# Optimization experiments

Hardware: AMD Instinct MI355X
Metric: run time of the kernel (lower is better)

## Reference

```python
import jax, jax.numpy as jnp
import numpy as np

EPS = 1e-5

def setup_inputs() -> dict:
    key = jax.random.key(0)
    ks = jax.random.split(key, 6)
    B, S, F, D = 512, 64, 768, 256
    # xavier-ish scales for weights
    return {
        "audio_feat": jax.random.normal(ks[0], (B, S, F), dtype=jnp.float32),
        "visual_feat": jax.random.normal(ks[1], (B, S, F), dtype=jnp.float32),
        "Wa": jax.random.normal(ks[2], (F, D), dtype=jnp.float32) * (1.0 / np.sqrt(F)),
        "ba": jnp.zeros((D,), dtype=jnp.float32),
        "Wv": jax.random.normal(ks[3], (F, D), dtype=jnp.float32) * (1.0 / np.sqrt(F)),
        "bv": jnp.zeros((D,), dtype=jnp.float32),
        "corr": jax.random.normal(ks[4], (D, D), dtype=jnp.float32) * float(np.sqrt(2.0 / (D + D))),
        "Wb": jax.random.normal(ks[5], (2 * D, 64), dtype=jnp.float32) * (1.0 / np.sqrt(2 * D)),
        "bb": jnp.zeros((64,), dtype=jnp.float32),
        "gamma": jnp.ones((64,), dtype=jnp.float32),
        "beta": jnp.zeros((64,), dtype=jnp.float32),
    }


def reference(audio_feat, visual_feat, Wa, ba, Wv, bv, corr, Wb, bb, gamma, beta):
    # project: [b,s,768] -> [b,s,256]
    a = jnp.einsum('bsf,fd->bsd', audio_feat, Wa) + ba      # audio proj
    v = jnp.einsum('bsf,fd->bsd', visual_feat, Wv) + bv     # vision proj
    vT = jnp.swapaxes(v, 1, 2)                              # [b,d,s]
    # bilinear correlation: cc[b,i,j] = a[b,i,:] @ corr @ v[b,j,:]
    cc = jnp.einsum('bid,de,bje->bij', a, corr, v)          # [b,sa,sv]
    audio_att = jax.nn.softmax(cc, axis=1)                  # softmax over audio positions
    visual_att = jax.nn.softmax(cc, axis=2)                 # softmax over visual positions (of cc^T along dim 1)
    # attended features, both [b,d,s]
    att_a = jnp.einsum('bid,bij->bdj', a, audio_att) + jnp.swapaxes(a, 1, 2)
    att_v = jnp.einsum('bdj,bij->bdi', vT, jnp.swapaxes(visual_att, 1, 2))
    # note: bmm(vT [b,d,sv], visual_att^T' ...) -> torch does vT @ visual_att_t where
    # visual_att_t[b,j,i] = visual_att[b,i,j]; equivalent einsum below
    att_v = jnp.einsum('bdj,bji->bdi', vT, jnp.swapaxes(visual_att, 1, 2)) + vT
    fused = jnp.concatenate([att_a, att_v], axis=1)         # [b,2d,s]
    fused = jnp.swapaxes(fused, 1, 2)                       # [b,s,2d]
    h = jnp.einsum('bsk,ko->bso', fused, Wb) + bb           # [b,s,64]
    mu = jnp.mean(h, axis=-1, keepdims=True)
    var = jnp.mean(jnp.square(h - mu), axis=-1, keepdims=True)
    h = (h - mu) * jax.lax.rsqrt(var + EPS) * gamma + beta
    return jax.nn.relu(h)
```

## Files before the change

### kernel.cpp

```cpp
#include <hip/hip_runtime.h>

typedef _Float16 f16x8 __attribute__((ext_vector_type(8)));
typedef _Float16 f16x4 __attribute__((ext_vector_type(4)));
typedef float    f32x4 __attribute__((ext_vector_type(4)));

#define A16_OFF   0u
#define V16_OFF   16777216u
#define WAP_OFF   33554432u
#define WVP_OFF   33947648u
#define CORRT_OFF 34340864u
#define WBT_OFF   34471936u

#define SCHED0() __builtin_amdgcn_sched_barrier(0)
#define SBAR()   __builtin_amdgcn_s_barrier()
#define LGKM0()  do { asm volatile("s_waitcnt lgkmcnt(0)" ::: "memory"); SCHED0(); } while (0)

__device__ __forceinline__ void gl_lds16(const void* g, void* l) {
    __builtin_amdgcn_global_load_lds(
        (const __attribute__((address_space(1))) void*)g,
        (__attribute__((address_space(3))) void*)l, 16, 0, 0);
}

__device__ __forceinline__ void vwait(int n) {
    switch (n) {
        case 0: asm volatile("s_waitcnt vmcnt(0)" ::: "memory"); break;
        case 4: asm volatile("s_waitcnt vmcnt(4)" ::: "memory"); break;
        case 8: asm volatile("s_waitcnt vmcnt(8)" ::: "memory"); break;
        default: asm volatile("s_waitcnt vmcnt(0)" ::: "memory"); break;
    }
}

__global__ __launch_bounds__(256) void k_prep(
    const float* __restrict__ Wa, const float* __restrict__ Wv,
    const float* __restrict__ corr, const float* __restrict__ Wb,
    _Float16* __restrict__ WaP, _Float16* __restrict__ WvP,
    _Float16* __restrict__ corrT, _Float16* __restrict__ WbT)
{
    __shared__ _Float16 tile[64][72];
    int bid = blockIdx.x;
    int t = threadIdx.x;
    if (bid < 192) {
        int z = bid >= 96;
        int b = z ? bid - 96 : bid;
        const float* W = z ? Wv : Wa;
        _Float16* P = z ? WvP : WaP;
        int kc = b >> 2, nbg = b & 3;
        int l = t & 63, sub = t >> 6;
        int nb = nbg * 4 + sub;
        int q = l >> 4, lm = l & 15;
        int k0 = kc * 32 + q * 8;
        int n = nb * 16 + lm;
        _Float16 tmp[8];
        #pragma unroll
        for (int e = 0; e < 8; ++e)
            tmp[e] = (_Float16)W[(size_t)(k0 + e) * 256 + n];
        *reinterpret_cast<f16x8*>(P + ((size_t)(kc * 16 + nb) * 64 + l) * 8) =
            *reinterpret_cast<const f16x8*>(tmp);
    } else {
        int b2 = bid - 192;
        const float* src; _Float16* dst; int R, C, tr, tc;
        if (b2 < 16) { src = corr; dst = corrT; R = 256; C = 256; tr = b2 >> 2; tc = b2 & 3; }
        else         { src = Wb;   dst = WbT;   R = 512; C = 64;  tr = b2 - 16; tc = 0;      }
        int r0 = tr * 64, c0 = tc * 64;
        #pragma unroll
        for (int it = 0; it < 16; ++it) {
            int idx = t + it * 256;
            int r = idx >> 6, c = idx & 63;
            tile[r][c] = (_Float16)src[(size_t)(r0 + r) * C + (c0 + c)];
        }
        __syncthreads();
        #pragma unroll
        for (int it = 0; it < 16; ++it) {
            int idx = t + it * 256;
            int c = idx >> 6, r = idx & 63;
            dst[(size_t)(c0 + c) * R + (r0 + r)] = tile[r][c];
        }
    }
}

__global__ __launch_bounds__(512, 1) void k_proj(
    const float* __restrict__ Xa, const float* __restrict__ Xv,
    const _Float16* __restrict__ WaP, const _Float16* __restrict__ WvP,
    const float* __restrict__ ba, const float* __restrict__ bv,
    _Float16* __restrict__ Aout, _Float16* __restrict__ Vout)
{
    extern __shared__ __align__(16) char smem[];

    const int bid = blockIdx.x;
    const int lin = (bid & 7) * 64 + (bid >> 3);
    const int z = lin >> 8, mb = lin & 255;
    const float*    X    = z ? Xv  : Xa;
    const _Float16* WP   = z ? WvP : WaP;
    const float*    bias = z ? bv  : ba;
    _Float16*       Out  = z ? Vout : Aout;
    const int m0 = mb * 128;

    const int t = threadIdx.x, lane = t & 63, w = t >> 6;
    const int wr = w >> 1, wc = w & 1;
    const int q = lane >> 4, lm = lane & 15;

    const float* Xb = X + (size_t)m0 * 768;

    f32x4 acc[2][8] = {};
    f32x4 sA[4], sB[4];

    auto loadA = [&](int ks, f32x4* s) {
        #pragma unroll
        for (int j = 0; j < 4; ++j) {
            int idx = j * 512 + t;
            int row = idx >> 4, c = idx & 15;
            s[j] = *reinterpret_cast<const f32x4*>(Xb + (size_t)row * 768 + ks * 64 + c * 4);
        }
    };
    auto writeA = [&](int buf, f32x4* s) {
        #pragma unroll
        for (int j = 0; j < 4; ++j) {
            int idx = j * 512 + t;
            int row = idx >> 4, c = idx & 15;
            int cs = c ^ ((row & 7) << 1);
            *reinterpret_cast<f32x4*>(smem + buf * 32768 + row * 256 + cs * 16) = s[j];
        }
    };
    auto stageB = [&](int ks, int buf) {
        char* base = smem + 65536 + buf * 32768;
        #pragma unroll
        for (int it = 0; it < 4; ++it) {
            int u0 = it * 512 + w * 64;
            gl_lds16(WP + ((size_t)ks * 2048 + u0 + lane) * 8, base + u0 * 16);
        }
    };

    loadA(0, sA); loadA(1, sB);
    stageB(0, 0); stageB(1, 1);
    vwait(8); SCHED0();
    writeA(0, sA); writeA(1, sB);
    loadA(2, sA);
    vwait(8); SCHED0();
    LGKM0();
    SBAR();

    #pragma unroll
    for (int ks = 0; ks < 12; ++ks) {
        const int cur = ks & 1;
        const char* Ac = smem + cur * 32768;
        const char* Bc = smem + 65536 + cur * 32768;

        f16x8 af[2][2];
        #pragma unroll
        for (int mf = 0; mf < 2; ++mf) {
            int rr = wr * 32 + mf * 16 + lm;
            #pragma unroll
            for (int kk = 0; kk < 2; ++kk) {
                int c0 = kk * 8 + 2 * q;
                int cs0 = c0 ^ ((rr & 7) << 1);
                int cs1 = (c0 + 1) ^ ((rr & 7) << 1);
                f32x4 lo = *reinterpret_cast<const f32x4*>(Ac + rr * 256 + cs0 * 16);
                f32x4 hi = *reinterpret_cast<const f32x4*>(Ac + rr * 256 + cs1 * 16);
                f16x4 l4 = __builtin_convertvector(lo, f16x4);
                f16x4 h4 = __builtin_convertvector(hi, f16x4);
                af[mf][kk] = __builtin_shufflevector(l4, h4, 0, 1, 2, 3, 4, 5, 6, 7);
            }
        }
        #pragma unroll
        for (int kk = 0; kk < 2; ++kk)
            #pragma unroll
            for (int nf = 0; nf < 8; ++nf) {
                int nb = wc * 8 + nf;
                f16x8 bf = *reinterpret_cast<const f16x8*>(
                    Bc + (kk * 1024 + nb * 64 + lane) * 16);
                acc[0][nf] = __builtin_amdgcn_mfma_f32_16x16x32_f16(af[0][kk], bf, acc[0][nf], 0, 0, 0);
                acc[1][nf] = __builtin_amdgcn_mfma_f32_16x16x32_f16(af[1][kk], bf, acc[1][nf], 0, 0, 0);
            }
        LGKM0();
        SBAR();

        if (ks + 2 < 12) stageB(ks + 2, cur);
        if (ks + 3 < 12) loadA(ks + 3, (ks & 1) ? sA : sB);
        if (ks + 2 < 12) {
            if (ks <= 8) vwait(8); else vwait(4);
            SCHED0();
            writeA(cur, (ks & 1) ? sB : sA);
        } else if (ks == 10) {
            vwait(0); SCHED0();
        }
        if (ks < 11) SBAR();
    }

    float biasv[8];
    #pragma unroll
    for (int nf = 0; nf < 8; ++nf)
        biasv[nf] = bias[wc * 128 + nf * 16 + lm];

    _Float16* Cs = (_Float16*)smem;
    #pragma unroll
    for (int mf = 0; mf < 2; ++mf)
        #pragma unroll
        for (int nf = 0; nf < 8; ++nf)
            #pragma unroll
            for (int r = 0; r < 4; ++r)
                Cs[(wr * 32 + mf * 16 + q * 4 + r) * 256 + wc * 128 + nf * 16 + lm] =
                    (_Float16)(acc[mf][nf][r] + biasv[nf]);
    __syncthreads();
    #pragma unroll
    for (int it = 0; it < 8; ++it) {
        int idx = t + it * 512;
        int row = idx >> 5, c = idx & 31;
        f16x8 vv = *reinterpret_cast<const f16x8*>(Cs + row * 256 + c * 8);
        *reinterpret_cast<f16x8*>(Out + (size_t)(m0 + row) * 256 + c * 8) = vv;
    }
}

#define SM_A    0u
#define SM_V    33792u
#define SM_AC   67584u
#define SM_CC   101376u
#define SM_ATA  118272u
#define SM_ATV  127488u
#define SM_AWT  136704u
#define SM_VWT  145920u
#define SM_RED  155136u
#define SM_TOTAL 159232u

__global__ __launch_bounds__(256) void k_fuse(
    const _Float16* __restrict__ A16, const _Float16* __restrict__ V16,
    const _Float16* __restrict__ corrT, const _Float16* __restrict__ WbT,
    const float* __restrict__ bb, const float* __restrict__ gamma,
    const float* __restrict__ beta, float* __restrict__ out)
{
    extern __shared__ char sm[];
    _Float16* a_s   = (_Float16*)(sm + SM_A);
    _Float16* v_s   = (_Float16*)(sm + SM_V);
    _Float16* ac_s  = (_Float16*)(sm + SM_AC);
    float*    cc_s  = (float*)(sm + SM_CC);
    _Float16* attAT = (_Float16*)(sm + SM_ATA);
    _Float16* attV  = (_Float16*)(sm + SM_ATV);
    _Float16* awT   = (_Float16*)(sm + SM_AWT);
    _Float16* vwT   = (_Float16*)(sm + SM_VWT);
    float*    red   = (float*)(sm + SM_RED);

    const int b = blockIdx.x;
    const int t = threadIdx.x, lane = t & 63, w = t >> 6;
    const int q = lane >> 4, lm = lane & 15;

    const _Float16* Ab = A16 + (size_t)b * 64 * 256;
    const _Float16* Vb = V16 + (size_t)b * 64 * 256;
    #pragma unroll
    for (int it = 0; it < 8; ++it) {
        int idx = t + it * 256;
        int row = idx >> 5, kc = idx & 31;
        *reinterpret_cast<f16x8*>(a_s + row * 264 + kc * 8) =
            *reinterpret_cast<const f16x8*>(Ab + row * 256 + kc * 8);
        *reinterpret_cast<f16x8*>(v_s + row * 264 + kc * 8) =
            *reinterpret_cast<const f16x8*>(Vb + row * 256 + kc * 8);
    }
    __syncthreads();

    {
        f32x4 acc[4][4] = {};
        for (int ks = 0; ks < 8; ++ks) {
            f16x8 af[4];
            #pragma unroll
            for (int mf = 0; mf < 4; ++mf)
                af[mf] = *reinterpret_cast<const f16x8*>(a_s + (mf * 16 + lm) * 264 + ks * 32 + q * 8);
            #pragma unroll
            for (int nf = 0; nf < 4; ++nf) {
                int e = w * 64 + nf * 16 + lm;
                f16x8 bf = *reinterpret_cast<const f16x8*>(corrT + (size_t)e * 256 + ks * 32 + q * 8);
                #pragma unroll
                for (int mf = 0; mf < 4; ++mf)
                    acc[mf][nf] = __builtin_amdgcn_mfma_f32_16x16x32_f16(af[mf], bf, acc[mf][nf], 0, 0, 0);
            }
        }
        #pragma unroll
        for (int mf = 0; mf < 4; ++mf)
            #pragma unroll
            for (int nf = 0; nf < 4; ++nf)
                #pragma unroll
                for (int r = 0; r < 4; ++r)
                    ac_s[(mf * 16 + 4 * q + r) * 264 + (w * 64 + nf * 16 + lm)] = (_Float16)acc[mf][nf][r];
    }
    __syncthreads();

    {
        f32x4 acc[4] = {};
        for (int ks = 0; ks < 8; ++ks) {
            f16x8 bf = *reinterpret_cast<const f16x8*>(v_s + (w * 16 + lm) * 264 + ks * 32 + q * 8);
            #pragma unroll
            for (int mf = 0; mf < 4; ++mf) {
                f16x8 af = *reinterpret_cast<const f16x8*>(ac_s + (mf * 16 + lm) * 264 + ks * 32 + q * 8);
                acc[mf] = __builtin_amdgcn_mfma_f32_16x16x32_f16(af, bf, acc[mf], 0, 0, 0);
            }
        }
        #pragma unroll
        for (int mf = 0; mf < 4; ++mf)
            #pragma unroll
            for (int r = 0; r < 4; ++r)
                cc_s[(mf * 16 + 4 * q + r) * 66 + (w * 16 + lm)] = acc[mf][r];
    }
    __syncthreads();

    {
        int j = t & 63, seg = w;
        float cmx = -1e30f, rmx = -1e30f;
        #pragma unroll
        for (int k = 0; k < 16; ++k) {
            int i = seg * 16 + k;
            cmx = fmaxf(cmx, cc_s[i * 66 + j]);
            rmx = fmaxf(rmx, cc_s[j * 66 + i]);
        }
        red[0 * 256 + seg * 64 + j] = cmx;
        red[2 * 256 + seg * 64 + j] = rmx;
        __syncthreads();
        float cm = fmaxf(fmaxf(red[0 * 256 + 0 * 64 + j], red[0 * 256 + 1 * 64 + j]),
                         fmaxf(red[0 * 256 + 2 * 64 + j], red[0 * 256 + 3 * 64 + j]));
        float rm = fmaxf(fmaxf(red[2 * 256 + 0 * 64 + j], red[2 * 256 + 1 * 64 + j]),
                         fmaxf(red[2 * 256 + 2 * 64 + j], red[2 * 256 + 3 * 64 + j]));
        float cs = 0.f, rs = 0.f;
        #pragma unroll
        for (int k = 0; k < 16; ++k) {
            int i = seg * 16 + k;
            cs += __expf(cc_s[i * 66 + j] - cm);
            rs += __expf(cc_s[j * 66 + i] - rm);
        }
        red[1 * 256 + seg * 64 + j] = cs;
        red[3 * 256 + seg * 64 + j] = rs;
        __syncthreads();
        float csum = red[1 * 256 + 0 * 64 + j] + red[1 * 256 + 1 * 64 + j] +
                     red[1 * 256 + 2 * 64 + j] + red[1 * 256 + 3 * 64 + j];
        float rsum = red[3 * 256 + 0 * 64 + j] + red[3 * 256 + 1 * 64 + j] +
                     red[3 * 256 + 2 * 64 + j] + red[3 * 256 + 3 * 64 + j];
        float cinv = 1.f / csum, rinv = 1.f / rsum;
        #pragma unroll
        for (int k = 0; k < 16; ++k) {
            int i = seg * 16 + k;
            float pa = __expf(cc_s[i * 66 + j] - cm) * cinv;
            if (i == j) pa += 1.f;
            attAT[j * 72 + i] = (_Float16)pa;
            float pv = __expf(cc_s[j * 66 + i] - rm) * rinv;
            if (i == j) pv += 1.f;
            attV[j * 72 + i] = (_Float16)pv;
        }
    }

    {
        int isV = w >> 1, wcol = w & 1;
        const _Float16* src = isV ? v_s : a_s;
        const int doff = isV ? 256 : 0;
        f32x4 acc[4][2] = {};
        for (int ks = 0; ks < 8; ++ks) {
            f16x8 af[4];
            #pragma unroll
            for (int mf = 0; mf < 4; ++mf)
                af[mf] = *reinterpret_cast<const f16x8*>(src + (mf * 16 + lm) * 264 + ks * 32 + q * 8);
            #pragma unroll
            for (int nf = 0; nf < 2; ++nf) {
                int o = wcol * 32 + nf * 16 + lm;
                f16x8 bf = *reinterpret_cast<const f16x8*>(WbT + (size_t)o * 512 + doff + ks * 32 + q * 8);
                #pragma unroll
                for (int mf = 0; mf < 4; ++mf)
                    acc[mf][nf] = __builtin_amdgcn_mfma_f32_16x16x32_f16(af[mf], bf, acc[mf][nf], 0, 0, 0);
            }
        }
        _Float16* dst = isV ? vwT : awT;
        #pragma unroll
        for (int mf = 0; mf < 4; ++mf)
            #pragma unroll
            for (int nf = 0; nf < 2; ++nf)
                #pragma unroll
                for (int r = 0; r < 4; ++r)
                    dst[(wcol * 32 + nf * 16 + lm) * 72 + (mf * 16 + 4 * q + r)] = (_Float16)acc[mf][nf][r];
    }
    __syncthreads();

    f32x4 hacc[4] = {};
    #pragma unroll
    for (int kk = 0; kk < 2; ++kk) {
        f16x8 a1 = *reinterpret_cast<const f16x8*>(attAT + (16 * w + lm) * 72 + kk * 32 + q * 8);
        f16x8 a2 = *reinterpret_cast<const f16x8*>(attV  + (16 * w + lm) * 72 + kk * 32 + q * 8);
        #pragma unroll
        for (int nf = 0; nf < 4; ++nf) {
            f16x8 b1 = *reinterpret_cast<const f16x8*>(awT + (nf * 16 + lm) * 72 + kk * 32 + q * 8);
            f16x8 b2 = *reinterpret_cast<const f16x8*>(vwT + (nf * 16 + lm) * 72 + kk * 32 + q * 8);
            hacc[nf] = __builtin_amdgcn_mfma_f32_16x16x32_f16(a1, b1, hacc[nf], 0, 0, 0);
            hacc[nf] = __builtin_amdgcn_mfma_f32_16x16x32_f16(a2, b2, hacc[nf], 0, 0, 0);
        }
    }

    {
        float bbv[4], gv[4], bev[4];
        #pragma unroll
        for (int nf = 0; nf < 4; ++nf) {
            int o = nf * 16 + lm;
            bbv[nf] = bb[o]; gv[nf] = gamma[o]; bev[nf] = beta[o];
        }
        #pragma unroll
        for (int r = 0; r < 4; ++r) {
            float vals[4]; float s1 = 0.f, s2 = 0.f;
            #pragma unroll
            for (int nf = 0; nf < 4; ++nf) {
                float hv = hacc[nf][r] + bbv[nf];
                vals[nf] = hv; s1 += hv; s2 += hv * hv;
            }
            #pragma unroll
            for (int m = 1; m < 16; m <<= 1) {
                s1 += __shfl_xor(s1, m, 64);
                s2 += __shfl_xor(s2, m, 64);
            }
            float mu = s1 * 0.015625f;
            float var = s2 * 0.015625f - mu * mu;
            float rstd = rsqrtf(var + 1e-5f);
            int s = 16 * w + 4 * q + r;
            float* orow = out + ((size_t)b * 64 + s) * 64;
            #pragma unroll
            for (int nf = 0; nf < 4; ++nf) {
                float y = (vals[nf] - mu) * rstd * gv[nf] + bev[nf];
                orow[nf * 16 + lm] = fmaxf(y, 0.f);
            }
        }
    }
}

extern "C" void kernel_launch(void* const* d_in, const int* in_sizes, int n_in,
                              void* d_out, int out_size, void* d_ws, size_t ws_size,
                              hipStream_t stream) {
    const float* Xa    = (const float*)d_in[0];
    const float* Xv    = (const float*)d_in[1];
    const float* Wa    = (const float*)d_in[2];
    const float* ba    = (const float*)d_in[3];
    const float* Wv    = (const float*)d_in[4];
    const float* bv    = (const float*)d_in[5];
    const float* corr  = (const float*)d_in[6];
    const float* Wb    = (const float*)d_in[7];
    const float* bb    = (const float*)d_in[8];
    const float* gamma = (const float*)d_in[9];
    const float* beta  = (const float*)d_in[10];
    float* out = (float*)d_out;
    char* ws = (char*)d_ws;

    _Float16* a16   = (_Float16*)(ws + A16_OFF);
    _Float16* v16   = (_Float16*)(ws + V16_OFF);
    _Float16* WaP   = (_Float16*)(ws + WAP_OFF);
    _Float16* WvP   = (_Float16*)(ws + WVP_OFF);
    _Float16* corrT = (_Float16*)(ws + CORRT_OFF);
    _Float16* WbT   = (_Float16*)(ws + WBT_OFF);

    hipLaunchKernelGGL(k_prep, dim3(216), dim3(256), 0, stream,
                       Wa, Wv, corr, Wb, WaP, WvP, corrT, WbT);
    (void)hipFuncSetAttribute((const void*)k_proj,
                              hipFuncAttributeMaxDynamicSharedMemorySize, 131072);
    hipLaunchKernelGGL(k_proj, dim3(512), dim3(512), 131072, stream,
                       Xa, Xv, WaP, WvP, ba, bv, a16, v16);
    (void)hipFuncSetAttribute((const void*)k_fuse,
                              hipFuncAttributeMaxDynamicSharedMemorySize, SM_TOTAL);
    hipLaunchKernelGGL(k_fuse, dim3(512), dim3(256), SM_TOTAL, stream,
                       a16, v16, corrT, WbT, bb, gamma, beta, out);
}
```

Before: 99.24 us.

## Restructure projection GEMM to 256-row tiles with register-direct A loads

The projection kernel now gives each block 256 rows, with each wave owning 32 full rows across all 256 output columns, so only 256 blocks launch. Activation tiles are loaded straight from global memory into registers in MFMA fragment layout, dropping the LDS staging, swizzle and writeback for A. Weights are staged into LDS in 192-wide K chunks with barriers around each chunk. This targets LDS traffic and halves repeated weight staging per row, at the cost of more registers (32 accumulators), less latency hiding for the weight loads, and half as many blocks on the device.

```diff
diff --git a/kernel.cpp b/kernel.cpp
--- a/kernel.cpp
+++ b/kernel.cpp
@@ -13,7 +13,6 @@
 
 #define SCHED0() __builtin_amdgcn_sched_barrier(0)
 #define SBAR()   __builtin_amdgcn_s_barrier()
-#define LGKM0()  do { asm volatile("s_waitcnt lgkmcnt(0)" ::: "memory"); SCHED0(); } while (0)
 
 __device__ __forceinline__ void gl_lds16(const void* g, void* l) {
     __builtin_amdgcn_global_load_lds(
@@ -24,7 +23,6 @@
 __device__ __forceinline__ void vwait(int n) {
     switch (n) {
         case 0: asm volatile("s_waitcnt vmcnt(0)" ::: "memory"); break;
-        case 4: asm volatile("s_waitcnt vmcnt(4)" ::: "memory"); break;
         case 8: asm volatile("s_waitcnt vmcnt(8)" ::: "memory"); break;
         default: asm volatile("s_waitcnt vmcnt(0)" ::: "memory"); break;
     }
@@ -87,126 +85,106 @@
     extern __shared__ __align__(16) char smem[];
 
     const int bid = blockIdx.x;
-    const int lin = (bid & 7) * 64 + (bid >> 3);
-    const int z = lin >> 8, mb = lin & 255;
+    const int lin = (bid & 7) * 32 + (bid >> 3);
+    const int z = lin >> 7, mb = lin & 127;
     const float*    X    = z ? Xv  : Xa;
     const _Float16* WP   = z ? WvP : WaP;
     const float*    bias = z ? bv  : ba;
     _Float16*       Out  = z ? Vout : Aout;
-    const int m0 = mb * 128;
+    const int m0 = mb * 256;
 
     const int t = threadIdx.x, lane = t & 63, w = t >> 6;
-    const int wr = w >> 1, wc = w & 1;
     const int q = lane >> 4, lm = lane & 15;
 
-    const float* Xb = X + (size_t)m0 * 768;
-
-    f32x4 acc[2][8] = {};
-    f32x4 sA[4], sB[4];
-
-    auto loadA = [&](int ks, f32x4* s) {
-        #pragma unroll
-        for (int j = 0; j < 4; ++j) {
-            int idx = j * 512 + t;
-            int row = idx >> 4, c = idx & 15;
-            s[j] = *reinterpret_cast<const f32x4*>(Xb + (size_t)row * 768 + ks * 64 + c * 4);
-        }
+    const float* Xw = X + (size_t)(m0 + w * 32) * 768;
+
+    f32x4 acc[2][16] = {};
+    f32x4 ra[8], rb[8];
+
+    auto loadA = [&](int k0, f32x4* s) {
+        #pragma unroll
+        for (int mf = 0; mf < 2; ++mf)
+            #pragma unroll
+            for (int kk = 0; kk < 2; ++kk)
+                #pragma unroll
+                for (int h = 0; h < 2; ++h)
+                    s[mf * 4 + kk * 2 + h] = *reinterpret_cast<const f32x4*>(
+                        Xw + (size_t)(mf * 16 + lm) * 768 + k0 + kk * 32 + q * 8 + h * 4);
     };
-    auto writeA = [&](int buf, f32x4* s) {
-        #pragma unroll
-        for (int j = 0; j < 4; ++j) {
-            int idx = j * 512 + t;
-            int row = idx >> 4, c = idx & 15;
-            int cs = c ^ ((row & 7) << 1);
-            *reinterpret_cast<f32x4*>(smem + buf * 32768 + row * 256 + cs * 16) = s[j];
+    auto stageB = [&](int c) {
+        #pragma unroll
+        for (int it = 0; it < 12; ++it) {
+            int u0 = it * 512 + w * 64;
+            gl_lds16(WP + ((size_t)c * 6144 + u0 + lane) * 8, smem + u0 * 16);
         }
     };
-    auto stageB = [&](int ks, int buf) {
-        char* base = smem + 65536 + buf * 32768;
-        #pragma unroll
-        for (int it = 0; it < 4; ++it) {
-            int u0 = it * 512 + w * 64;
-            gl_lds16(WP + ((size_t)ks * 2048 + u0 + lane) * 8, base + u0 * 16);
-        }
-    };
-
-    loadA(0, sA); loadA(1, sB);
-    stageB(0, 0); stageB(1, 1);
-    vwait(8); SCHED0();
-    writeA(0, sA); writeA(1, sB);
-    loadA(2, sA);
-    vwait(8); SCHED0();
-    LGKM0();
-    SBAR();
 
     #pragma unroll
-    for (int ks = 0; ks < 12; ++ks) {
-        const int cur = ks & 1;
-        const char* Ac = smem + cur * 32768;
-        const char* Bc = smem + 65536 + cur * 32768;
-
-        f16x8 af[2][2];
-        #pragma unroll
-        for (int mf = 0; mf < 2; ++mf) {
-            int rr = wr * 32 + mf * 16 + lm;
+    for (int c = 0; c < 4; ++c) {
+        const int k0 = c * 192;
+        SBAR();
+        stageB(c);
+        loadA(k0, ra);
+        vwait(8); SCHED0();
+        SBAR();
+
+        #pragma unroll
+        for (int s = 0; s < 3; ++s) {
+            f32x4* cur = (s & 1) ? rb : ra;
+            f32x4* nxt = (s & 1) ? ra : rb;
+            if (s < 2) loadA(k0 + (s + 1) * 64, nxt);
+            vwait(s < 2 ? 8 : 0); SCHED0();
+            f16x8 af[2][2];
+            #pragma unroll
+            for (int mf = 0; mf < 2; ++mf)
+                #pragma unroll
+                for (int kk = 0; kk < 2; ++kk) {
+                    f16x4 l4 = __builtin_convertvector(cur[mf * 4 + kk * 2], f16x4);
+                    f16x4 h4 = __builtin_convertvector(cur[mf * 4 + kk * 2 + 1], f16x4);
+                    af[mf][kk] = __builtin_shufflevector(l4, h4, 0, 1, 2, 3, 4, 5, 6, 7);
+                }
             #pragma unroll
             for (int kk = 0; kk < 2; ++kk) {
-                int c0 = kk * 8 + 2 * q;
-                int cs0 = c0 ^ ((rr & 7) << 1);
-                int cs1 = (c0 + 1) ^ ((rr & 7) << 1);
-                f32x4 lo = *reinterpret_cast<const f32x4*>(Ac + rr * 256 + cs0 * 16);
-                f32x4 hi = *reinterpret_cast<const f32x4*>(Ac + rr * 256 + cs1 * 16);
-                f16x4 l4 = __builtin_convertvector(lo, f16x4);
-                f16x4 h4 = __builtin_convertvector(hi, f16x4);
-                af[mf][kk] = __builtin_shufflevector(l4, h4, 0, 1, 2, 3, 4, 5, 6, 7);
-            }
-        }
-        #pragma unroll
-        for (int kk = 0; kk < 2; ++kk)
-            #pragma unroll
-            for (int nf = 0; nf < 8; ++nf) {
-                int nb = wc * 8 + nf;
-                f16x8 bf = *reinterpret_cast<const f16x8*>(
-                    Bc + (kk * 1024 + nb * 64 + lane) * 16);
-                acc[0][nf] = __builtin_amdgcn_mfma_f32_16x16x32_f16(af[0][kk], bf, acc[0][nf], 0, 0, 0);
-                acc[1][nf] = __builtin_amdgcn_mfma_f32_16x16x32_f16(af[1][kk], bf, acc[1][nf], 0, 0, 0);
-            }
-        LGKM0();
-        SBAR();
-
-        if (ks + 2 < 12) stageB(ks + 2, cur);
-        if (ks + 3 < 12) loadA(ks + 3, (ks & 1) ? sA : sB);
-        if (ks + 2 < 12) {
-            if (ks <= 8) vwait(8); else vwait(4);
-            SCHED0();
-            writeA(cur, (ks & 1) ? sB : sA);
-        } else if (ks == 10) {
-            vwait(0); SCHED0();
-        }
-        if (ks < 11) SBAR();
-    }
-
-    float biasv[8];
+                const int kcl = s * 2 + kk;
+                #pragma unroll
+                for (int nf = 0; nf < 16; ++nf) {
+                    f16x8 bf = *reinterpret_cast<const f16x8*>(
+                        smem + (((kcl * 16 + nf) * 64) + lane) * 16);
+                    acc[0][nf] = __builtin_amdgcn_mfma_f32_16x16x32_f16(af[0][kk], bf, acc[0][nf], 0, 0, 0);
+                    acc[1][nf] = __builtin_amdgcn_mfma_f32_16x16x32_f16(af[1][kk], bf, acc[1][nf], 0, 0, 0);
+                }
+            }
+        }
+    }
+
+    float biasv[16];
     #pragma unroll
-    for (int nf = 0; nf < 8; ++nf)
-        biasv[nf] = bias[wc * 128 + nf * 16 + lm];
+    for (int nf = 0; nf < 16; ++nf)
+        biasv[nf] = bias[nf * 16 + lm];
 
     _Float16* Cs = (_Float16*)smem;
     #pragma unroll
-    for (int mf = 0; mf < 2; ++mf)
-        #pragma unroll
-        for (int nf = 0; nf < 8; ++nf)
-            #pragma unroll
-            for (int r = 0; r < 4; ++r)
-                Cs[(wr * 32 + mf * 16 + q * 4 + r) * 256 + wc * 128 + nf * 16 + lm] =
-                    (_Float16)(acc[mf][nf][r] + biasv[nf]);
-    __syncthreads();
-    #pragma unroll
-    for (int it = 0; it < 8; ++it) {
-        int idx = t + it * 512;
-        int row = idx >> 5, c = idx & 31;
-        f16x8 vv = *reinterpret_cast<const f16x8*>(Cs + row * 256 + c * 8);
-        *reinterpret_cast<f16x8*>(Out + (size_t)(m0 + row) * 256 + c * 8) = vv;
+    for (int h = 0; h < 2; ++h) {
+        __syncthreads();
+        if ((w >> 2) == h) {
+            int rbase = (w & 3) * 32;
+            #pragma unroll
+            for (int mf = 0; mf < 2; ++mf)
+                #pragma unroll
+                for (int nf = 0; nf < 16; ++nf)
+                    #pragma unroll
+                    for (int r = 0; r < 4; ++r)
+                        Cs[(rbase + mf * 16 + q * 4 + r) * 256 + nf * 16 + lm] =
+                            (_Float16)(acc[mf][nf][r] + biasv[nf]);
+        }
+        __syncthreads();
+        #pragma unroll
+        for (int it = 0; it < 8; ++it) {
+            int idx = t + it * 512;
+            int row = idx >> 5, c8 = idx & 31;
+            f16x8 vv = *reinterpret_cast<const f16x8*>(Cs + row * 256 + c8 * 8);
+            *reinterpret_cast<f16x8*>(Out + (size_t)(m0 + h * 128 + row) * 256 + c8 * 8) = vv;
+        }
     }
 }
 
@@ -447,8 +425,8 @@
     hipLaunchKernelGGL(k_prep, dim3(216), dim3(256), 0, stream,
                        Wa, Wv, corr, Wb, WaP, WvP, corrT, WbT);
     (void)hipFuncSetAttribute((const void*)k_proj,
-                              hipFuncAttributeMaxDynamicSharedMemorySize, 131072);
-    hipLaunchKernelGGL(k_proj, dim3(512), dim3(512), 131072, stream,
+                              hipFuncAttributeMaxDynamicSharedMemorySize, 98304);
+    hipLaunchKernelGGL(k_proj, dim3(256), dim3(512), 98304, stream,
                        Xa, Xv, WaP, WvP, ba, bv, a16, v16);
     (void)hipFuncSetAttribute((const void*)k_fuse,
                               hipFuncAttributeMaxDynamicSharedMemorySize, SM_TOTAL);
```

Result: slower. 103.2 us (+4.0%).
